# Performance work log

Measured on AMD Instinct MI355X. Metric: run time of the kernel, lower is better.

## Reference

```python
import jax, jax.numpy as jnp
import numpy as np

EPS = 1e-6
NEG = 0.2  # leaky-relu negative slope
OBJ_C = 6

def _knn(x, k):
    # x: [B,3,N] -> [B,N,k] indices of k nearest neighbors (incl. self)
    xx = jnp.sum(x * x, axis=1)
    inner = jnp.einsum('bdn,bdm->bnm', x, x)
    pd = 2.0 * inner - xx[:, :, None] - xx[:, None, :]  # negative sq dist
    return jax.lax.top_k(pd, k)[1]

def _gather_pts(xt, idx):
    # xt [B,N,D], idx [B,N,k] -> [B,N,k,D]
    return xt[jnp.arange(xt.shape[0])[:, None, None], idx]

def _vn_lin(W, x):
    # channel-mixing linear over VN channel dim: x [B,Cin,3,...]
    return jnp.einsum('oc,bc...->bo...', W, x)

def _vn_bn(x, g, b, eps=1e-5):
    # VNBatchNorm with batch statistics on vector norms
    n = jnp.linalg.norm(x, axis=2) + EPS          # [B,C,*spatial]
    axes = (0,) + tuple(range(2, n.ndim))
    m = jnp.mean(n, axes, keepdims=True)
    v = jnp.var(n, axes, keepdims=True)
    shp = (1, -1) + (1,) * (n.ndim - 2)
    nb = g.reshape(shp) * (n - m) / jnp.sqrt(v + eps) + b.reshape(shp)
    return x / n[:, :, None] * nb[:, :, None]

def _vn_leaky(p, d):
    dot = jnp.sum(p * d, axis=2, keepdims=True)
    dsq = jnp.sum(d * d, axis=2, keepdims=True)
    return NEG * p + (1.0 - NEG) * jnp.where(dot >= 0, p, p - (dot / (dsq + EPS)) * d)

def _vn_block(x, wf, wd, g=None, b=None):
    # VNLinearLeakyReLU
    p = _vn_lin(wf, x)
    if g is not None:
        p = _vn_bn(p, g, b)
    return _vn_leaky(p, _vn_lin(wd, x))

def _surface_feature(coord, k):
    # coord [B,3,N] -> [B,3(chan),3(vec),N,k]: (nb-ctr, ctr, nb x ctr)
    idx = _knn(coord, k)
    xt = coord.transpose(0, 2, 1)                                  # [B,N,3]
    nb = _gather_pts(xt, idx)[:, :, :, None, :]                    # [B,N,k,1,3]
    ctr = jnp.broadcast_to(xt[:, :, None, None, :], nb.shape)
    f = jnp.concatenate([nb - ctr, ctr, jnp.cross(nb, ctr, axis=-1)], axis=3)
    return f.transpose(0, 3, 4, 1, 2)

def _neighbor_feature(x, coord, k):
    # x [B,C,3,N], knn over coord -> [B,C,3,N,k]
    B, C, _, N = x.shape
    idx = _knn(coord, k)
    xt = x.reshape(B, C * 3, N).transpose(0, 2, 1)                 # [B,N,C*3]
    f = _gather_pts(xt, idx).reshape(B, N, k, C, 3)
    return f.transpose(0, 3, 4, 1, 2)

def _vn_maxpool_down(x, coord, wd, rate):
    # x [B,C,3,N,k]: stride-subsample points, VN-max over k neighbors
    x = x[:, :, :, ::rate, :]
    coord_d = coord[:, :, ::rate]
    dot = jnp.sum(x * _vn_lin(wd, x), axis=2)                      # [B,C,Nd,k]
    idx = jnp.argmax(dot, axis=-1)
    xm = jnp.take_along_axis(x, idx[:, :, None, :, None], axis=-1)[..., 0]
    return xm, coord_d

def _nearest_index(t, s):
    # t [B,N,3], s [B,M,3] -> argmin sq-dist index [B,N]
    d = jnp.sum(t * t, -1)[:, :, None] - 2.0 * jnp.einsum('bnd,bmd->bnm', t, s) + jnp.sum(s * s, -1)[:, None, :]
    return jnp.argmin(d, axis=-1)

def _index_points(x, idx):
    # x [B,C,3,M], idx [B,N] -> [B,C,3,N]
    xt = x.transpose(0, 3, 1, 2)
    return xt[jnp.arange(x.shape[0])[:, None], idx].transpose(0, 2, 3, 1)

def _conv_bn_relu(x, w, b, g, be, eps=1e-5):
    # 1x1 Conv1d + BatchNorm1d (batch stats) + ReLU
    y = jnp.einsum('oc,bcn->bon', w, x) + b[None, :, None]
    m = jnp.mean(y, (0, 2), keepdims=True)
    v = jnp.var(y, (0, 2), keepdims=True)
    return jax.nn.relu(g[None, :, None] * (y - m) / jnp.sqrt(v + eps) + be[None, :, None])

def _forward(x, norm, cat_id, wf0, wd0, g0, b0, wf1, wd1, g1, b1, wp1, wf2, wd2, g2, b2, wf3, wd3, g3, b3, wp2, wf4, wd4, g4, b4, wv1f, wv1d, wv2f, wv2d, w3, ws1, cb1, sg1, sb1, ws2, cb2, sg2, sb2, ws3, cb3, sg3, sb3):
    B, _, _, N = x.shape
    coord = x.reshape(B, 3, N)
    one_hot = jax.nn.one_hot(cat_id, OBJ_C, dtype=x.dtype)
    x0 = _vn_block(_surface_feature(coord, 20), wf0, wd0, g0, b0).mean(-1)   # [B,42,3,N]
    x1 = _vn_block(x0, wf1, wd1, g1, b1)
    x2, coord2 = _vn_maxpool_down(_neighbor_feature(x1, coord, 4), coord, wp1, 4)
    x2 = _vn_block(x2, wf2, wd2, g2, b2)                                     # [B,84,3,N/4]
    x3 = _vn_block(x2, wf3, wd3, g3, b3)
    x4, coord4 = _vn_maxpool_down(_neighbor_feature(x3, coord2, 4), coord2, wp2, 4)
    x4 = _vn_block(x4, wf4, wd4, g4, b4)                                     # [B,168,3,N/16]
    ct = coord.transpose(0, 2, 1)
    i1 = _nearest_index(ct, coord2.transpose(0, 2, 1))
    i2 = _nearest_index(ct, coord4.transpose(0, 2, 1))
    eqv = jnp.concatenate([x0, x1, _index_points(x2, i1), _index_points(x3, i1), _index_points(x4, i2)], axis=1)  # [B,420,3,N]
    mean_feat = eqv.mean(-1, keepdims=True)                                  # [B,420,3,1]
    z = _vn_block(mean_feat, wv1f, wv1d)
    z = _vn_block(z, wv2f, wv2d)
    z = jnp.einsum('bcvm,kc->bvkm', z, w3)                                   # [B,3,2,1]
    inv_gl = jnp.einsum('bijm,bjkm->bikm', mean_feat, z).reshape(B, -1, 1)   # [B,840,1]
    inv_0 = jnp.broadcast_to(inv_gl, (B, inv_gl.shape[1], N))
    inv_1 = jnp.sum(mean_feat * coord[:, None], axis=2)                      # [B,420,N]
    oh = jnp.broadcast_to(one_hot[:, :, None], (B, OBJ_C, N))
    inv = jnp.concatenate([norm, inv_0, inv_1, oh], axis=1)                  # [B,1267,N]
    inv = _conv_bn_relu(inv, ws1, cb1, sg1, sb1)
    inv = _conv_bn_relu(inv, ws2, cb2, sg2, sb2)
    inv = _conv_bn_relu(inv, ws3, cb3, sg3, sb3)                             # [B,420,N]
    return eqv, mean_feat, inv, inv_gl

def setup_inputs():
    key = jax.random.key(0)
    ki = iter(jax.random.split(key, 40))
    B, N, D = 4, 2048, 42
    def lin(o, c):
        return jax.random.normal(next(ki), (o, c), jnp.float32) / float(np.sqrt(c))
    inp = dict(
        x=jax.random.normal(next(ki), (B, 1, 3, N), jnp.float32),
        norm=jax.random.normal(next(ki), (B, 1, N), jnp.float32),
        cat_id=jax.random.randint(next(ki), (B,), 0, OBJ_C),
        wf0=lin(D, 3), wd0=lin(D, 3), g0=jnp.ones(D), b0=jnp.zeros(D),
        wf1=lin(D, D), wd1=lin(D, D), g1=jnp.ones(D), b1=jnp.zeros(D),
        wp1=lin(D, D),
        wf2=lin(2 * D, D), wd2=lin(2 * D, D), g2=jnp.ones(2 * D), b2=jnp.zeros(2 * D),
        wf3=lin(2 * D, 2 * D), wd3=lin(2 * D, 2 * D), g3=jnp.ones(2 * D), b3=jnp.zeros(2 * D),
        wp2=lin(2 * D, 2 * D),
        wf4=lin(4 * D, 2 * D), wd4=lin(4 * D, 2 * D), g4=jnp.ones(4 * D), b4=jnp.zeros(4 * D),
        wv1f=lin(5 * D, 10 * D), wv1d=lin(5 * D, 10 * D),
        wv2f=lin(2 * D, 5 * D), wv2d=lin(2 * D, 5 * D),
        w3=lin(2, 2 * D),
        ws1=lin(1024, 1267), cb1=jnp.zeros(1024), sg1=jnp.ones(1024), sb1=jnp.zeros(1024),
        ws2=lin(512, 1024), cb2=jnp.zeros(512), sg2=jnp.ones(512), sb2=jnp.zeros(512),
        ws3=lin(420, 512), cb3=jnp.zeros(420), sg3=jnp.ones(420), sb3=jnp.zeros(420),
    )
    return inp

def reference(x, norm, cat_id, wf0, wd0, g0, b0, wf1, wd1, g1, b1, wp1, wf2, wd2, g2, b2, wf3, wd3, g3, b3, wp2, wf4, wd4, g4, b4, wv1f, wv1d, wv2f, wv2d, w3, ws1, cb1, sg1, sb1, ws2, cb2, sg2, sb2, ws3, cb3, sg3, sb3):
    return _forward(x, norm, cat_id, wf0, wd0, g0, b0, wf1, wd1, g1, b1, wp1, wf2, wd2, g2, b2, wf3, wd3, g3, b3, wp2, wf4, wd4, g4, b4, wv1f, wv1d, wv2f, wv2d, w3, ws1, cb1, sg1, sb1, ws2, cb2, sg2, sb2, ws3, cb3, sg3, sb3)
```

## Files before the change

kernel.cpp:

```cpp
#include <hip/hip_runtime.h>
#include <hip/hip_bf16.h>
#include <cstdint>
#include <cstddef>

#define NTOT 2048
#define BTOT 4

typedef short bf16x8 __attribute__((ext_vector_type(8)));
typedef float f32x4 __attribute__((ext_vector_type(4)));

__device__ inline unsigned short f2b(float v) {
    __hip_bfloat16 h = __float2bfloat16(v);
    return *reinterpret_cast<unsigned short*>(&h);
}

static const size_t WS_IDX20 = 0;
static const size_t WS_X0    = 1638400;
static const size_t WS_X1    = 3702784;
static const size_t WS_XM2   = 5767168;
static const size_t WS_X2    = 6025216;
static const size_t WS_X3    = 6541312;
static const size_t WS_IDX42 = 7057408;
static const size_t WS_XM4   = 7059456;
static const size_t WS_X4    = 7188480;
static const size_t WS_I1    = 7446528;
static const size_t WS_I2    = 7454720;
static const size_t WS_MF    = 7462912;
static const size_t WS_INVGL = 7467952;
static const size_t WS_STATS = 7471312;
static const size_t WS_CST   = 7472992;
static const size_t WS_CB    = 7480320;
static const size_t WS_AB    = 7484416;
static const size_t WS_W0    = 7496704;
static const size_t WS_Z1    = 7497728;
static const size_t WS_Z2    = 7500288;
static const size_t WS_W2B   = 13378560;
static const size_t WS_W3B   = 13640704;
static const size_t WS_Y1B   = 0;
static const size_t WS_Y2T   = 7480320;
static const size_t WS_Y2B   = 4194304;
static const size_t WS_Y3T   = 13771776;

#define ZERO_SPAN_BYTES ((7476904 - 7462912) * 4)

#define ST0_OFF 0
#define ST1_OFF 84
#define ST2_OFF 168
#define ST3_OFF 336
#define ST4_OFF 504
#define CST1_OFF 0
#define CST2_OFF 2048
#define CST3_OFF 3072

#define OUT_EQV   0
#define OUT_MF    10321920
#define OUT_INV   10326960
#define OUT_INVGL 13767600

template <int SLOTS, int K, int NQ>
__global__ __launch_bounds__(256)
void knn_reg_kernel(const float* __restrict__ coord, int cand_stride, int q_stride,
                    int* __restrict__ out_idx, int q_cnt)
{
#pragma clang fp contract(off)
    constexpr int Q = SLOTS / 8;
    int b = blockIdx.y;
    int wave = threadIdx.x >> 6, lane = threadIdx.x & 63;
    int qbase = (blockIdx.x * 4 + wave) * NQ;
    if (qbase >= q_cnt) return;
    float qx[NQ], qy[NQ], qz[NQ], xxq[NQ];
#pragma unroll
    for (int u = 0; u < NQ; ++u) {
        int nq = (qbase + u) * q_stride;
        qx[u] = coord[(b * 3 + 0) * NTOT + nq];
        qy[u] = coord[(b * 3 + 1) * NTOT + nq];
        qz[u] = coord[(b * 3 + 2) * NTOT + nq];
        xxq[u] = qx[u] * qx[u] + qy[u] * qy[u] + qz[u] * qz[u];
    }
    float v[NQ][SLOTS];
#pragma unroll
    for (int j = 0; j < SLOTS; ++j) {
        int mo = (lane + 64 * j) * cand_stride;
        float cx = coord[(b * 3 + 0) * NTOT + mo];
        float cy = coord[(b * 3 + 1) * NTOT + mo];
        float cz = coord[(b * 3 + 2) * NTOT + mo];
        float xxc = cx * cx + cy * cy + cz * cz;
#pragma unroll
        for (int u = 0; u < NQ; ++u) {
            float inner = qx[u] * cx + qy[u] * cy + qz[u] * cz;
            v[u][j] = (2.0f * inner - xxq[u]) - xxc;
        }
    }
    float qv[NQ][Q]; int qj[NQ][Q];
#pragma unroll
    for (int u = 0; u < NQ; ++u)
#pragma unroll
        for (int qq = 0; qq < Q; ++qq) {
            float nv = v[u][qq * 8]; int nj = qq * 8;
#pragma unroll
            for (int j = 1; j < 8; ++j)
                if (v[u][qq * 8 + j] > nv) { nv = v[u][qq * 8 + j]; nj = qq * 8 + j; }
            qv[u][qq] = nv; qj[u][qq] = nj;
        }
#pragma clang loop unroll(disable)
    for (int kk = 0; kk < K; ++kk) {
        float bv[NQ]; int bm[NQ];
#pragma unroll
        for (int u = 0; u < NQ; ++u) {
            float tv = qv[u][0]; int tj = qj[u][0];
#pragma unroll
            for (int qq = 1; qq < Q; ++qq)
                if (qv[u][qq] > tv) { tv = qv[u][qq]; tj = qj[u][qq]; }
            bv[u] = tv; bm[u] = lane + 64 * tj;
        }
        for (int off = 32; off; off >>= 1) {
            float ov[NQ]; int om[NQ];
#pragma unroll
            for (int u = 0; u < NQ; ++u) {
                ov[u] = __shfl_down(bv[u], off);
                om[u] = __shfl_down(bm[u], off);
            }
#pragma unroll
            for (int u = 0; u < NQ; ++u)
                if (ov[u] > bv[u] || (ov[u] == bv[u] && om[u] < bm[u])) {
                    bv[u] = ov[u]; bm[u] = om[u];
                }
        }
#pragma unroll
        for (int u = 0; u < NQ; ++u) {
            int m_win = __builtin_amdgcn_readfirstlane(bm[u]);
            if (lane == 0)
                out_idx[((size_t)(b * q_cnt) + qbase + u) * K + kk] = m_win;
            int w_slot = m_win >> 6;
            bool isw = (lane == (m_win & 63));
#pragma unroll
            for (int qq = 0; qq < Q; ++qq) {
                if (qq == (w_slot >> 3)) {
#pragma unroll
                    for (int j = 0; j < 8; ++j)
                        if (qq * 8 + j == w_slot)
                            v[u][qq * 8 + j] = isw ? -3.4e38f : v[u][qq * 8 + j];
                    float nv = v[u][qq * 8]; int nj = qq * 8;
#pragma unroll
                    for (int j = 1; j < 8; ++j)
                        if (v[u][qq * 8 + j] > nv) { nv = v[u][qq * 8 + j]; nj = qq * 8 + j; }
                    qv[u][qq] = nv; qj[u][qq] = nj;
                }
            }
        }
    }
}

template <int SLOTS>
__global__ __launch_bounds__(256)
void nearest_reg_kernel(const float* __restrict__ coord, int cand_stride,
                        int* __restrict__ out)
{
#pragma clang fp contract(off)
    int b = blockIdx.y;
    int wave = threadIdx.x >> 6, lane = threadIdx.x & 63;
    int n = blockIdx.x * 4 + wave;
    float qx = coord[(b * 3 + 0) * NTOT + n];
    float qy = coord[(b * 3 + 1) * NTOT + n];
    float qz = coord[(b * 3 + 2) * NTOT + n];
    float tt = qx * qx + qy * qy + qz * qz;
    float v[SLOTS];
#pragma unroll
    for (int j = 0; j < SLOTS; ++j) {
        int mo = (lane + 64 * j) * cand_stride;
        float cx = coord[(b * 3 + 0) * NTOT + mo];
        float cy = coord[(b * 3 + 1) * NTOT + mo];
        float cz = coord[(b * 3 + 2) * NTOT + mo];
        float inner = qx * cx + qy * cy + qz * cz;
        float ss = cx * cx + cy * cy + cz * cz;
        v[j] = (tt - 2.0f * inner) + ss;
    }
    float bv = v[0];
    int bj = 0;
#pragma unroll
    for (int j = 1; j < SLOTS; ++j)
        if (v[j] < bv) { bv = v[j]; bj = j; }
    int bm = lane + 64 * bj;
    for (int off = 32; off; off >>= 1) {
        float ov = __shfl_down(bv, off);
        int   om = __shfl_down(bm, off);
        if (ov < bv || (ov == bv && om < bm)) { bv = ov; bm = om; }
    }
    if (lane == 0) out[b * NTOT + n] = bm;
}

__global__ __launch_bounds__(256)
void stats0_kernel(const float* __restrict__ coord, const int* __restrict__ idx20,
                   const float* __restrict__ wf0, double* __restrict__ stats)
{
    __shared__ float nbc[360];
    __shared__ float ctr[18];
    __shared__ double red[2][6][42];
    int t = threadIdx.x, b = blockIdx.y;
    int ps = t / 42, o = t - ps * 42;
    bool active = ps < 6;
    float w0 = 0.f, w1 = 0.f, w2 = 0.f;
    if (active) { w0 = wf0[o * 3]; w1 = wf0[o * 3 + 1]; w2 = wf0[o * 3 + 2]; }
    double s = 0.0, s2 = 0.0;
    int base = blockIdx.x * 48;
    for (int it = 0; it < 8; ++it) {
        int n0 = base + it * 6;
        __syncthreads();
        if (t < 120) {
            int pl = t / 20, k = t - pl * 20;
            int n = n0 + pl; if (n > NTOT - 1) n = NTOT - 1;
            int m = idx20[((size_t)(b * NTOT + n)) * 20 + k];
            nbc[t * 3 + 0] = coord[(b * 3 + 0) * NTOT + m];
            nbc[t * 3 + 1] = coord[(b * 3 + 1) * NTOT + m];
            nbc[t * 3 + 2] = coord[(b * 3 + 2) * NTOT + m];
        }
        if (t >= 128 && t < 146) {
            int i = t - 128; int pl = i / 3, vd = i - pl * 3;
            int n = n0 + pl; if (n > NTOT - 1) n = NTOT - 1;
            ctr[i] = coord[(b * 3 + vd) * NTOT + n];
        }
        __syncthreads();
        if (active && n0 + ps < NTOT) {
            float cx = ctr[ps * 3], cy = ctr[ps * 3 + 1], cz = ctr[ps * 3 + 2];
            const float* nb = &nbc[ps * 60];
            for (int k = 0; k < 20; ++k) {
                float nx = nb[k * 3], ny = nb[k * 3 + 1], nz = nb[k * 3 + 2];
                float dx = nx - cx, dy = ny - cy, dz = nz - cz;
                float crx = ny * cz - nz * cy;
                float cry = nz * cx - nx * cz;
                float crz = nx * cy - ny * cx;
                float p0 = w0 * dx + w1 * cx + w2 * crx;
                float p1 = w0 * dy + w1 * cy + w2 * cry;
                float p2 = w0 * dz + w1 * cz + w2 * crz;
                float nrm = sqrtf(p0 * p0 + p1 * p1 + p2 * p2) + 1e-6f;
                s += (double)nrm; s2 += (double)nrm * (double)nrm;
            }
        }
    }
    if (active) { red[0][ps][o] = s; red[1][ps][o] = s2; }
    __syncthreads();
    if (t < 42) {
        double a = 0.0, a2 = 0.0;
#pragma unroll
        for (int p = 0; p < 6; ++p) { a += red[0][p][t]; a2 += red[1][p][t]; }
        atomicAdd(&stats[t], a);
        atomicAdd(&stats[42 + t], a2);
    }
}

__global__ __launch_bounds__(256)
void apply0_kernel(const float* __restrict__ coord, const int* __restrict__ idx20,
                   const float* __restrict__ wf0, const float* __restrict__ wd0,
                   const float* __restrict__ g0, const float* __restrict__ b0,
                   const double* __restrict__ stats, float* __restrict__ x0)
{
    __shared__ float nbc[360];
    __shared__ float ctr[18];
    int t = threadIdx.x;
    int b = blockIdx.y;
    int ps = t / 42, o = t - ps * 42;
    int n0 = blockIdx.x * 6;
    if (t < 120) {
        int pl = t / 20, k = t - pl * 20;
        int n = n0 + pl; if (n > NTOT - 1) n = NTOT - 1;
        int m = idx20[((size_t)(b * NTOT + n)) * 20 + k];
        nbc[t * 3 + 0] = coord[(b * 3 + 0) * NTOT + m];
        nbc[t * 3 + 1] = coord[(b * 3 + 1) * NTOT + m];
        nbc[t * 3 + 2] = coord[(b * 3 + 2) * NTOT + m];
    }
    if (t >= 128 && t < 146) {
        int i = t - 128; int pl = i / 3, vd = i - pl * 3;
        int n = n0 + pl; if (n > NTOT - 1) n = NTOT - 1;
        ctr[i] = coord[(b * 3 + vd) * NTOT + n];
    }
    __syncthreads();
    int n = n0 + ps;
    if (ps >= 6 || n >= NTOT) return;
    double S1 = stats[o], S2 = stats[42 + o];
    double md = S1 / 163840.0;
    float m = (float)md;
    float var = (float)(S2 / 163840.0 - md * md);
    float gs = g0[o] / sqrtf(var + 1e-5f);
    float bb = b0[o];
    float wa0 = wf0[o * 3], wa1 = wf0[o * 3 + 1], wa2 = wf0[o * 3 + 2];
    float wb0 = wd0[o * 3], wb1 = wd0[o * 3 + 1], wb2 = wd0[o * 3 + 2];
    float cx = ctr[ps * 3], cy = ctr[ps * 3 + 1], cz = ctr[ps * 3 + 2];
    const float* nb = &nbc[ps * 60];
    float a0 = 0.f, a1 = 0.f, a2 = 0.f;
    for (int k = 0; k < 20; ++k) {
        float nx = nb[k * 3], ny = nb[k * 3 + 1], nz = nb[k * 3 + 2];
        float dx = nx - cx, dy = ny - cy, dz = nz - cz;
        float crx = ny * cz - nz * cy;
        float cry = nz * cx - nx * cz;
        float crz = nx * cy - ny * cx;
        float p0 = wa0 * dx + wa1 * cx + wa2 * crx;
        float p1 = wa0 * dy + wa1 * cy + wa2 * cry;
        float p2 = wa0 * dz + wa1 * cz + wa2 * crz;
        float d0 = wb0 * dx + wb1 * cx + wb2 * crx;
        float d1 = wb0 * dy + wb1 * cy + wb2 * cry;
        float d2 = wb0 * dz + wb1 * cz + wb2 * crz;
        float nrm = sqrtf(p0 * p0 + p1 * p1 + p2 * p2) + 1e-6f;
        float nbv = gs * (nrm - m) + bb;
        float sc = nbv / nrm;
        p0 *= sc; p1 *= sc; p2 *= sc;
        float dot = p0 * d0 + p1 * d1 + p2 * d2;
        float dsq = d0 * d0 + d1 * d1 + d2 * d2 + 1e-6f;
        float tq = fminf(dot, 0.f) / dsq;
        a0 += 0.2f * p0 + 0.8f * (p0 - tq * d0);
        a1 += 0.2f * p1 + 0.8f * (p1 - tq * d1);
        a2 += 0.2f * p2 + 0.8f * (p2 - tq * d2);
    }
    x0[((size_t)(b * 42 + o) * 3 + 0) * NTOT + n] = a0 / 20.0f;
    x0[((size_t)(b * 42 + o) * 3 + 1) * NTOT + n] = a1 / 20.0f;
    x0[((size_t)(b * 42 + o) * 3 + 2) * NTOT + n] = a2 / 20.0f;
}

template <int Ci, int Co, int PTS, int NT, int NIT>
__global__ __launch_bounds__(NT)
void vn_stats_kernel(const float* __restrict__ xin,
                     const float* __restrict__ wf,
                     double* __restrict__ stats, int Npts)
{
    constexpr int Ci3 = Ci * 3;
    constexpr int STRIDE = Ci3 + 1;
    __shared__ float col[PTS * STRIDE];
    __shared__ double red[2][PTS][Co];
    int t = threadIdx.x;
    int b = blockIdx.y;
    int ps = t / Co;
    int o = t - ps * Co;
    bool active = ps < PTS;
    double s = 0.0, s2 = 0.0;
    int base = blockIdx.x * (PTS * NIT);
    for (int it = 0; it < NIT; ++it) {
        int pt0 = base + it * PTS;
        __syncthreads();
        for (int i = t; i < PTS * Ci3; i += NT) {
            int pl = i / Ci3, off = i - pl * Ci3;
            int pt = pt0 + pl; if (pt >= Npts) pt = Npts - 1;
            col[pl * STRIDE + off] = xin[(size_t)(b * 3 * Ci + off) * Npts + pt];
        }
        __syncthreads();
        if (active && pt0 + ps < Npts) {
            const float* cl = &col[ps * STRIDE];
            const float* wr = wf + o * Ci;
            float p0 = 0.f, p1 = 0.f, p2 = 0.f;
#pragma unroll
            for (int c = 0; c < Ci; ++c) {
                float w = wr[c];
                p0 += w * cl[3 * c]; p1 += w * cl[3 * c + 1]; p2 += w * cl[3 * c + 2];
            }
            float nrm = sqrtf(p0 * p0 + p1 * p1 + p2 * p2) + 1e-6f;
            s += (double)nrm; s2 += (double)nrm * (double)nrm;
        }
    }
    if (active) { red[0][ps][o] = s; red[1][ps][o] = s2; }
    __syncthreads();
    if (t < Co) {
        double a = 0.0, a2 = 0.0;
#pragma unroll
        for (int p = 0; p < PTS; ++p) { a += red[0][p][t]; a2 += red[1][p][t]; }
        atomicAdd(&stats[t], a);
        atomicAdd(&stats[Co + t], a2);
    }
}

template <int Ci, int Co, int PTS, int NT>
__global__ __launch_bounds__(NT)
void vn_apply_kernel(const float* __restrict__ xin,
                     const float* __restrict__ wf,
                     const float* __restrict__ wd,
                     const float* __restrict__ g,
                     const float* __restrict__ bbp,
                     const double* __restrict__ stats,
                     double count, int Npts,
                     float* __restrict__ xout)
{
    constexpr int Ci3 = Ci * 3;
    constexpr int STRIDE = Ci3 + 1;
    __shared__ float col[PTS * STRIDE];
    int t = threadIdx.x;
    int b = blockIdx.y;
    int ps = t / Co;
    int o = t - ps * Co;
    bool active = ps < PTS;
    float m = 0.f, gs = 0.f, bb = 0.f;
    if (active) {
        double S1 = stats[o], S2 = stats[Co + o];
        double md = S1 / count;
        m = (float)md;
        float var = (float)(S2 / count - md * md);
        gs = g[o] / sqrtf(var + 1e-5f);
        bb = bbp[o];
    }
    int pt0 = blockIdx.x * PTS;
    for (int i = t; i < PTS * Ci3; i += NT) {
        int pl = i / Ci3, off = i - pl * Ci3;
        int pt = pt0 + pl; if (pt >= Npts) pt = Npts - 1;
        col[pl * STRIDE + off] = xin[(size_t)(b * 3 * Ci + off) * Npts + pt];
    }
    __syncthreads();
    int pt = pt0 + ps;
    if (!active || pt >= Npts) return;
    const float* cl = &col[ps * STRIDE];
    const float* wr = wf + o * Ci;
    const float* wdr = wd + o * Ci;
    float p0 = 0.f, p1 = 0.f, p2 = 0.f, d0 = 0.f, d1 = 0.f, d2 = 0.f;
#pragma unroll
    for (int c = 0; c < Ci; ++c) {
        float c0 = cl[3 * c], c1 = cl[3 * c + 1], c2 = cl[3 * c + 2];
        float w = wr[c];
        p0 += w * c0; p1 += w * c1; p2 += w * c2;
        float w2 = wdr[c];
        d0 += w2 * c0; d1 += w2 * c1; d2 += w2 * c2;
    }
    float nrm = sqrtf(p0 * p0 + p1 * p1 + p2 * p2) + 1e-6f;
    float nb = gs * (nrm - m) + bb;
    float sc = nb / nrm;
    p0 *= sc; p1 *= sc; p2 *= sc;
    float dot = p0 * d0 + p1 * d1 + p2 * d2;
    float dsq = d0 * d0 + d1 * d1 + d2 * d2 + 1e-6f;
    float tq = fminf(dot, 0.f) / dsq;
    float r0 = p0 - tq * d0, r1 = p1 - tq * d1, r2 = p2 - tq * d2;
    xout[((size_t)(b * Co + o) * 3 + 0) * Npts + pt] = 0.2f * p0 + 0.8f * r0;
    xout[((size_t)(b * Co + o) * 3 + 1) * Npts + pt] = 0.2f * p1 + 0.8f * r1;
    xout[((size_t)(b * Co + o) * 3 + 2) * Npts + pt] = 0.2f * p2 + 0.8f * r2;
}

__global__ void vn_pool_kernel(const float* __restrict__ xin,
                               const int* __restrict__ idx, long long sb, int sq,
                               const float* __restrict__ wp,
                               float* __restrict__ xout,
                               int C, int Np, int Nq)
{
#pragma clang fp contract(off)
    __shared__ float nb[4 * 84 * 3];
    int b = blockIdx.y;
    int q = blockIdx.x;
    const int* ir = idx + b * sb + (long long)q * sq;
    for (int kk = 0; kk < 4; ++kk) {
        int mm = ir[kk];
        for (int t = threadIdx.x; t < C * 3; t += blockDim.x)
            nb[kk * C * 3 + t] = xin[(size_t)(b * 3 * C + t) * Np + mm];
    }
    __syncthreads();
    int o = threadIdx.x;
    if (o >= C) return;
    const float* wr = wp + o * C;
    float best = -3.4e38f;
    int bk = 0;
    for (int kk = 0; kk < 4; ++kk) {
        const float* cl = &nb[kk * C * 3];
        float d0 = 0.f, d1 = 0.f, d2 = 0.f;
        for (int c = 0; c < C; ++c) {
            float w = wr[c];
            d0 += w * cl[3 * c]; d1 += w * cl[3 * c + 1]; d2 += w * cl[3 * c + 2];
        }
        float dot = cl[o * 3] * d0 + cl[o * 3 + 1] * d1 + cl[o * 3 + 2] * d2;
        if (dot > best) { best = dot; bk = kk; }
    }
    const float* cb = &nb[bk * C * 3];
    xout[((size_t)(b * C + o) * 3 + 0) * Nq + q] = cb[o * 3];
    xout[((size_t)(b * C + o) * 3 + 1) * Nq + q] = cb[o * 3 + 1];
    xout[((size_t)(b * C + o) * 3 + 2) * Nq + q] = cb[o * 3 + 2];
}

__global__ void eqv_kernel(const float* __restrict__ x0, const float* __restrict__ x1,
                           const float* __restrict__ x2, const float* __restrict__ x3,
                           const float* __restrict__ x4,
                           const int* __restrict__ i1, const int* __restrict__ i2,
                           float* __restrict__ out_eqv, float* __restrict__ mfw)
{
    __shared__ float wsum[4];
    int n = blockIdx.x * 256 + threadIdx.x;
    int cv = blockIdx.y;
    int b = blockIdx.z;
    int cc = cv / 3, v = cv % 3;
    float val;
    if (cc < 42)
        val = x0[((size_t)(b * 42 + cc) * 3 + v) * NTOT + n];
    else if (cc < 84)
        val = x1[((size_t)(b * 42 + (cc - 42)) * 3 + v) * NTOT + n];
    else if (cc < 168) {
        int m = i1[b * NTOT + n];
        val = x2[((size_t)(b * 84 + (cc - 84)) * 3 + v) * 512 + m];
    } else if (cc < 252) {
        int m = i1[b * NTOT + n];
        val = x3[((size_t)(b * 84 + (cc - 168)) * 3 + v) * 512 + m];
    } else {
        int m = i2[b * NTOT + n];
        val = x4[((size_t)(b * 168 + (cc - 252)) * 3 + v) * 128 + m];
    }
    out_eqv[((size_t)(b * 1260 + cv)) * NTOT + n] = val;
    float s = val;
    for (int off = 32; off; off >>= 1) s += __shfl_down(s, off);
    if ((threadIdx.x & 63) == 0) wsum[threadIdx.x >> 6] = s;
    __syncthreads();
    if (threadIdx.x == 0)
        atomicAdd(&mfw[b * 1260 + cv], (wsum[0] + wsum[1]) + (wsum[2] + wsum[3]));
}

__global__ void mf_finalize_kernel(float* __restrict__ mfw, float* __restrict__ out_mf)
{
    int i = blockIdx.x * 256 + threadIdx.x;
    if (i < 5040) {
        float m = mfw[i] / 2048.0f;
        mfw[i] = m;
        out_mf[i] = m;
    }
}

__global__ __launch_bounds__(256)
void z1_kernel(const float* __restrict__ mfw,
               const float* __restrict__ wv1f, const float* __restrict__ wv1d,
               float* __restrict__ z1ws)
{
    __shared__ float mf[1260];
    int b = blockIdx.y;
    int wave = threadIdx.x >> 6, lane = threadIdx.x & 63;
    for (int i = threadIdx.x; i < 1260; i += 256) mf[i] = mfw[b * 1260 + i];
    __syncthreads();
    int o = blockIdx.x * 4 + wave;
    if (o >= 210) return;
    const float* wr  = wv1f + (size_t)o * 420;
    const float* wdr = wv1d + (size_t)o * 420;
    float p0 = 0.f, p1 = 0.f, p2 = 0.f, d0 = 0.f, d1 = 0.f, d2 = 0.f;
    for (int c = lane; c < 420; c += 64) {
        float m0 = mf[3 * c], m1 = mf[3 * c + 1], m2 = mf[3 * c + 2];
        float w = wr[c];
        p0 += w * m0; p1 += w * m1; p2 += w * m2;
        float w2 = wdr[c];
        d0 += w2 * m0; d1 += w2 * m1; d2 += w2 * m2;
    }
    for (int off = 32; off; off >>= 1) {
        p0 += __shfl_down(p0, off); p1 += __shfl_down(p1, off);
        p2 += __shfl_down(p2, off); d0 += __shfl_down(d0, off);
        d1 += __shfl_down(d1, off); d2 += __shfl_down(d2, off);
    }
    if (lane == 0) {
        float dot = p0 * d0 + p1 * d1 + p2 * d2;
        float r0, r1, r2;
        if (dot >= 0.f) { r0 = p0; r1 = p1; r2 = p2; }
        else {
            float tq = dot / (d0 * d0 + d1 * d1 + d2 * d2 + 1e-6f);
            r0 = p0 - tq * d0; r1 = p1 - tq * d1; r2 = p2 - tq * d2;
        }
        z1ws[b * 630 + o * 3]     = 0.2f * p0 + 0.8f * r0;
        z1ws[b * 630 + o * 3 + 1] = 0.2f * p1 + 0.8f * r1;
        z1ws[b * 630 + o * 3 + 2] = 0.2f * p2 + 0.8f * r2;
    }
}

__global__ __launch_bounds__(256)
void z2_kernel(const float* __restrict__ z1ws,
               const float* __restrict__ wv2f, const float* __restrict__ wv2d,
               float* __restrict__ z2ws)
{
    __shared__ float zl[630];
    int b = blockIdx.y;
    int wave = threadIdx.x >> 6, lane = threadIdx.x & 63;
    for (int i = threadIdx.x; i < 630; i += 256) zl[i] = z1ws[b * 630 + i];
    __syncthreads();
    int o = blockIdx.x * 4 + wave;
    if (o >= 84) return;
    const float* wr  = wv2f + (size_t)o * 210;
    const float* wdr = wv2d + (size_t)o * 210;
    float p0 = 0.f, p1 = 0.f, p2 = 0.f, d0 = 0.f, d1 = 0.f, d2 = 0.f;
    for (int c = lane; c < 210; c += 64) {
        float m0 = zl[3 * c], m1 = zl[3 * c + 1], m2 = zl[3 * c + 2];
        float w = wr[c];
        p0 += w * m0; p1 += w * m1; p2 += w * m2;
        float w2 = wdr[c];
        d0 += w2 * m0; d1 += w2 * m1; d2 += w2 * m2;
    }
    for (int off = 32; off; off >>= 1) {
        p0 += __shfl_down(p0, off); p1 += __shfl_down(p1, off);
        p2 += __shfl_down(p2, off); d0 += __shfl_down(d0, off);
        d1 += __shfl_down(d1, off); d2 += __shfl_down(d2, off);
    }
    if (lane == 0) {
        float dot = p0 * d0 + p1 * d1 + p2 * d2;
        float r0, r1, r2;
        if (dot >= 0.f) { r0 = p0; r1 = p1; r2 = p2; }
        else {
            float tq = dot / (d0 * d0 + d1 * d1 + d2 * d2 + 1e-6f);
            r0 = p0 - tq * d0; r1 = p1 - tq * d1; r2 = p2 - tq * d2;
        }
        z2ws[b * 252 + o * 3]     = 0.2f * p0 + 0.8f * r0;
        z2ws[b * 252 + o * 3 + 1] = 0.2f * p1 + 0.8f * r1;
        z2ws[b * 252 + o * 3 + 2] = 0.2f * p2 + 0.8f * r2;
    }
}

__global__ void z3invgl_kernel(const float* __restrict__ mfw,
                               const float* __restrict__ z2ws,
                               const float* __restrict__ w3,
                               float* __restrict__ invgl_ws,
                               float* __restrict__ out_invgl)
{
    __shared__ float z2[252];
    __shared__ float z3[6];
    __shared__ float mf[1260];
    int b = blockIdx.x;
    int t = threadIdx.x;
    for (int i = t; i < 252; i += 256) z2[i] = z2ws[b * 252 + i];
    for (int i = t; i < 1260; i += 256) mf[i] = mfw[b * 1260 + i];
    __syncthreads();
    if (t < 6) {
        int v = t / 2, kt = t % 2;
        float s = 0.f;
        for (int c = 0; c < 84; ++c) s += z2[c * 3 + v] * w3[kt * 84 + c];
        z3[v * 2 + kt] = s;
    }
    __syncthreads();
    for (int i = t; i < 840; i += 256) {
        int ii = i / 2, kt = i % 2;
        float s = mf[ii * 3] * z3[0 + kt] + mf[ii * 3 + 1] * z3[2 + kt] +
                  mf[ii * 3 + 2] * z3[4 + kt];
        invgl_ws[b * 840 + i] = s;
        out_invgl[b * 840 + i] = s;
    }
}

__global__ __launch_bounds__(256)
void conv1_coef_kernel(const float* __restrict__ ws1,
                       const float* __restrict__ invgl,
                       const float* __restrict__ mfw,
                       const int* __restrict__ cat,
                       float* __restrict__ cb, float* __restrict__ ab,
                       float* __restrict__ w0)
{
    int wave = threadIdx.x >> 6, lane = threadIdx.x & 63;
    int o = blockIdx.x * 4 + wave;
    int b = blockIdx.y;
    const float* wr = ws1 + (size_t)o * 1267;
    float s = 0.f;
    for (int j = lane; j < 840; j += 64)
        s += wr[1 + j] * invgl[b * 840 + j];
    float a0 = 0.f, a1 = 0.f, a2 = 0.f;
    for (int i = lane; i < 420; i += 64) {
        float w = wr[841 + i];
        a0 += w * mfw[b * 1260 + i * 3];
        a1 += w * mfw[b * 1260 + i * 3 + 1];
        a2 += w * mfw[b * 1260 + i * 3 + 2];
    }
    for (int off = 32; off; off >>= 1) {
        s  += __shfl_down(s, off);
        a0 += __shfl_down(a0, off);
        a1 += __shfl_down(a1, off);
        a2 += __shfl_down(a2, off);
    }
    if (lane == 0) {
        cb[b * 1024 + o] = s + wr[1261 + cat[b]];
        ab[((size_t)(b * 1024 + o)) * 3 + 0] = a0;
        ab[((size_t)(b * 1024 + o)) * 3 + 1] = a1;
        ab[((size_t)(b * 1024 + o)) * 3 + 2] = a2;
        if (b == 0) w0[o] = wr[0];
    }
}

__global__ __launch_bounds__(256)
void y1_stats_kernel(const float* __restrict__ cb, const float* __restrict__ ab,
                     const float* __restrict__ w0, const float* __restrict__ coord,
                     const float* __restrict__ normv, float* __restrict__ cst)
{
    __shared__ float px[256], py[256], pz[256], pn[256];
    int t = threadIdx.x;
    int o = blockIdx.x * 256 + t;
    int b = blockIdx.y >> 3;
    int n0 = (blockIdx.y & 7) * 256;
    px[t] = coord[(b * 3 + 0) * NTOT + n0 + t];
    py[t] = coord[(b * 3 + 1) * NTOT + n0 + t];
    pz[t] = coord[(b * 3 + 2) * NTOT + n0 + t];
    pn[t] = normv[b * NTOT + n0 + t];
    __syncthreads();
    size_t bo = (size_t)(b * 1024 + o);
    float c0 = cb[bo];
    float a0 = ab[bo * 3], a1 = ab[bo * 3 + 1], a2 = ab[bo * 3 + 2];
    float wn = w0[o];
    float s = 0.f, s2 = 0.f;
    for (int k = 0; k < 256; ++k) {
        float v = c0 + a0 * px[k] + a1 * py[k] + a2 * pz[k] + wn * pn[k];
        s += v; s2 += v * v;
    }
    atomicAdd(&cst[o], s);
    atomicAdd(&cst[1024 + o], s2);
}

__global__ __launch_bounds__(256)
void y1_bnrelu_kernel(const float* __restrict__ cb, const float* __restrict__ ab,
                      const float* __restrict__ w0, const float* __restrict__ coord,
                      const float* __restrict__ normv, const float* __restrict__ cst,
                      const float* __restrict__ sg, const float* __restrict__ sb,
                      unsigned short* __restrict__ y1b)
{
    __shared__ float px[256], py[256], pz[256], pn[256];
    int t = threadIdx.x;
    int o = blockIdx.x * 256 + t;
    int b = blockIdx.y >> 3;
    int n0 = (blockIdx.y & 7) * 256;
    px[t] = coord[(b * 3 + 0) * NTOT + n0 + t];
    py[t] = coord[(b * 3 + 1) * NTOT + n0 + t];
    pz[t] = coord[(b * 3 + 2) * NTOT + n0 + t];
    pn[t] = normv[b * NTOT + n0 + t];
    __syncthreads();
    size_t bo = (size_t)(b * 1024 + o);
    float c0 = cb[bo];
    float a0 = ab[bo * 3], a1 = ab[bo * 3 + 1], a2 = ab[bo * 3 + 2];
    float wn = w0[o];
    float mm = cst[o] * (1.f / 8192.f);
    float var = cst[1024 + o] * (1.f / 8192.f) - mm * mm;
    float sc = sg[o] / sqrtf(var + 1e-5f);
    float bs = sb[o] - mm * sc;
    size_t rowbase = (size_t)(b * NTOT + n0) * 1024 + o;
    for (int k = 0; k < 256; ++k) {
        float v = c0 + a0 * px[k] + a1 * py[k] + a2 * pz[k] + wn * pn[k];
        float r = sc * v + bs;
        y1b[rowbase + (size_t)k * 1024] = f2b(r > 0.f ? r : 0.f);
    }
}

__global__ void wconv_kernel(const float* __restrict__ src, unsigned short* __restrict__ dst,
                             int Msrc, int Ksrc, int Kpad)
{
    int k = blockIdx.x * 256 + threadIdx.x;
    int o = blockIdx.y;
    float v = (o < Msrc && k < Ksrc) ? src[(size_t)o * Ksrc + k] : 0.f;
    dst[(size_t)o * Kpad + k] = f2b(v);
}

__global__ __launch_bounds__(256)
void gemm_mfma_kernel(const unsigned short* __restrict__ A,
                      const unsigned short* __restrict__ Bw,
                      float* __restrict__ C, float* __restrict__ st,
                      int K, int Mreal)
{
    __shared__ __align__(16) unsigned short Al[64 * 72];
    __shared__ __align__(16) unsigned short Bl[64 * 72];
    __shared__ float sst[64], sst2[64];
    int t = threadIdx.x;
    if (t < 64) { sst[t] = 0.f; sst2[t] = 0.f; }
    int r0 = blockIdx.x * 64;
    int c0 = blockIdx.y * 64;
    int w = t >> 6, l = t & 63;
    int wm = w & 1, wn = w >> 1;
    int lm = l & 15, lq = l >> 4;
    f32x4 acc[2][2] = {};
    for (int k0 = 0; k0 < K; k0 += 64) {
#pragma unroll
        for (int half = 0; half < 2; ++half) {
            int ch = t + half * 256;
            int row = ch >> 3, kc = ch & 7;
            *(uint4*)&Al[row * 72 + kc * 8] =
                *(const uint4*)&A[(size_t)(r0 + row) * K + k0 + kc * 8];
            *(uint4*)&Bl[row * 72 + kc * 8] =
                *(const uint4*)&Bw[(size_t)(c0 + row) * K + k0 + kc * 8];
        }
        __syncthreads();
        bf16x8 af[2][2], bfr[2][2];
#pragma unroll
        for (int kk = 0; kk < 2; ++kk) {
#pragma unroll
            for (int i = 0; i < 2; ++i)
                af[kk][i] = *(const bf16x8*)&Al[(wm * 32 + i * 16 + lm) * 72 + kk * 32 + lq * 8];
#pragma unroll
            for (int j = 0; j < 2; ++j)
                bfr[kk][j] = *(const bf16x8*)&Bl[(wn * 32 + j * 16 + lm) * 72 + kk * 32 + lq * 8];
        }
#pragma unroll
        for (int kk = 0; kk < 2; ++kk)
#pragma unroll
            for (int i = 0; i < 2; ++i)
#pragma unroll
                for (int j = 0; j < 2; ++j)
                    acc[i][j] = __builtin_amdgcn_mfma_f32_16x16x32_bf16(
                        af[kk][i], bfr[kk][j], acc[i][j], 0, 0, 0);
        __syncthreads();
    }
#pragma unroll
    for (int i = 0; i < 2; ++i) {
#pragma unroll
        for (int j = 0; j < 2; ++j) {
            int col = c0 + wn * 32 + j * 16 + lm;
            if (col < Mreal) {
                int rbase = r0 + wm * 32 + i * 16 + lq * 4;
#pragma unroll
                for (int r = 0; r < 4; ++r)
                    C[(size_t)(rbase + r) * Mreal + col] = acc[i][j][r];
            }
        }
    }
#pragma unroll
    for (int j = 0; j < 2; ++j) {
        float s = 0.f, s2 = 0.f;
#pragma unroll
        for (int i = 0; i < 2; ++i)
#pragma unroll
            for (int r = 0; r < 4; ++r) { float x = acc[i][j][r]; s += x; s2 += x * x; }
        s  += __shfl_down(s, 32);  s  += __shfl_down(s, 16);
        s2 += __shfl_down(s2, 32); s2 += __shfl_down(s2, 16);
        if (l < 16) {
            int cc = wn * 32 + j * 16 + lm;
            atomicAdd(&sst[cc], s);
            atomicAdd(&sst2[cc], s2);
        }
    }
    __syncthreads();
    if (t < 64) {
        int col = c0 + t;
        if (col < Mreal) {
            atomicAdd(&st[col], sst[t]);
            atomicAdd(&st[Mreal + col], sst2[t]);
        }
    }
}

__global__ void bnreluT_kernel(const float* __restrict__ Ct, const float* __restrict__ st,
                               const float* __restrict__ g, const float* __restrict__ be,
                               unsigned short* __restrict__ outb, int M, int maskM)
{
    size_t idx = (size_t)blockIdx.x * 256 + threadIdx.x;
    int o = (int)(idx & (size_t)maskM);
    float m = st[o] * (1.f / 8192.f);
    float var = st[M + o] * (1.f / 8192.f) - m * m;
    float sqv = sqrtf(var + 1e-5f);
    float v = g[o] * (Ct[idx] - m) / sqv + be[o];
    outb[idx] = f2b(v > 0.f ? v : 0.f);
}

__global__ void bnrelu_outT_kernel(const float* __restrict__ Ct, const float* __restrict__ st,
                                   const float* __restrict__ g, const float* __restrict__ be,
                                   float* __restrict__ outinv)
{
    __shared__ float tile[64][65];
    int t = threadIdx.x;
    int r0 = blockIdx.x * 64;
    int o0 = blockIdx.y * 64;
    int b = r0 >> 11, n0 = r0 & 2047;
    int oi = t & 63;
    int o = o0 + oi;
    float m = 0.f, sqv = 1.f, gg = 0.f, bb = 0.f;
    if (o < 420) {
        m = st[o] * (1.f / 8192.f);
        float var = st[420 + o] * (1.f / 8192.f) - m * m;
        sqv = sqrtf(var + 1e-5f);
        gg = g[o]; bb = be[o];
    }
    for (int it = 0; it < 16; ++it) {
        int rr = it * 4 + (t >> 6);
        float v = 0.f;
        if (o < 420) {
            v = gg * (Ct[(size_t)(r0 + rr) * 420 + o] - m) / sqv + bb;
            v = v > 0.f ? v : 0.f;
        }
        tile[rr][oi] = v;
    }
    __syncthreads();
    for (int it = 0; it < 16; ++it) {
        int oc = it * 4 + (t >> 6);
        int oo = o0 + oc;
        if (oo < 420)
            outinv[((size_t)(b * 420 + oo)) * 2048 + n0 + (t & 63)] = tile[t & 63][oc];
    }
}

extern "C" void kernel_launch(void* const* d_in, const int* in_sizes, int n_in,
                              void* d_out, int out_size, void* d_ws, size_t ws_size,
                              hipStream_t stream)
{
    (void)in_sizes; (void)n_in; (void)out_size; (void)ws_size;
    const float* xc   = (const float*)d_in[0];
    const float* normv= (const float*)d_in[1];
    const int*   cat  = (const int*)d_in[2];
    const float* wf0  = (const float*)d_in[3];
    const float* wd0  = (const float*)d_in[4];
    const float* g0   = (const float*)d_in[5];
    const float* b0   = (const float*)d_in[6];
    const float* wf1  = (const float*)d_in[7];
    const float* wd1  = (const float*)d_in[8];
    const float* g1   = (const float*)d_in[9];
    const float* b1   = (const float*)d_in[10];
    const float* wp1  = (const float*)d_in[11];
    const float* wf2  = (const float*)d_in[12];
    const float* wd2  = (const float*)d_in[13];
    const float* g2   = (const float*)d_in[14];
    const float* b2   = (const float*)d_in[15];
    const float* wf3  = (const float*)d_in[16];
    const float* wd3  = (const float*)d_in[17];
    const float* g3   = (const float*)d_in[18];
    const float* b3   = (const float*)d_in[19];
    const float* wp2  = (const float*)d_in[20];
    const float* wf4  = (const float*)d_in[21];
    const float* wd4  = (const float*)d_in[22];
    const float* g4   = (const float*)d_in[23];
    const float* b4   = (const float*)d_in[24];
    const float* wv1f = (const float*)d_in[25];
    const float* wv1d = (const float*)d_in[26];
    const float* wv2f = (const float*)d_in[27];
    const float* wv2d = (const float*)d_in[28];
    const float* w3   = (const float*)d_in[29];
    const float* ws1  = (const float*)d_in[30];
    const float* sg1  = (const float*)d_in[32];
    const float* sb1  = (const float*)d_in[33];
    const float* ws2  = (const float*)d_in[34];
    const float* sg2  = (const float*)d_in[36];
    const float* sb2  = (const float*)d_in[37];
    const float* ws3  = (const float*)d_in[38];
    const float* sg3  = (const float*)d_in[40];
    const float* sb3  = (const float*)d_in[41];

    float* ws = (float*)d_ws;
    float* out = (float*)d_out;

    int*    idx20 = (int*)(ws + WS_IDX20);
    float*  x0    = ws + WS_X0;
    float*  x1    = ws + WS_X1;
    float*  xm2   = ws + WS_XM2;
    float*  x2    = ws + WS_X2;
    float*  x3    = ws + WS_X3;
    int*    idx42 = (int*)(ws + WS_IDX42);
    float*  xm4   = ws + WS_XM4;
    float*  x4    = ws + WS_X4;
    int*    i1p   = (int*)(ws + WS_I1);
    int*    i2p   = (int*)(ws + WS_I2);
    float*  mfw   = ws + WS_MF;
    float*  invgl = ws + WS_INVGL;
    double* st    = (double*)(ws + WS_STATS);
    float*  cst   = ws + WS_CST;
    float*  cb    = ws + WS_CB;
    float*  ab    = ws + WS_AB;
    float*  w0    = ws + WS_W0;
    float*  z1ws  = ws + WS_Z1;
    float*  z2ws  = ws + WS_Z2;
    unsigned short* w2b  = (unsigned short*)(ws + WS_W2B);
    unsigned short* w3b  = (unsigned short*)(ws + WS_W3B);
    unsigned short* y1b  = (unsigned short*)(ws + WS_Y1B);
    float*  y2t   = ws + WS_Y2T;
    unsigned short* y2b  = (unsigned short*)(ws + WS_Y2B);
    float*  y3t   = ws + WS_Y3T;

    hipMemsetAsync((void*)mfw, 0, ZERO_SPAN_BYTES, stream);

    wconv_kernel<<<dim3(4, 512), 256, 0, stream>>>(ws2, w2b, 512, 1024, 1024);
    wconv_kernel<<<dim3(2, 512), 256, 0, stream>>>(ws3, w3b, 420, 512, 512);

    knn_reg_kernel<32, 20, 2><<<dim3(256, 4), 256, 0, stream>>>(xc, 1, 1, idx20, 2048);

    stats0_kernel<<<dim3(43, 4), 256, 0, stream>>>(xc, idx20, wf0, st + ST0_OFF);
    apply0_kernel<<<dim3(342, 4), 256, 0, stream>>>(xc, idx20, wf0, wd0, g0, b0,
                                                    st + ST0_OFF, x0);

    vn_stats_kernel<42, 42, 6, 256, 8><<<dim3(43, 4), 256, 0, stream>>>(
        x0, wf1, st + ST1_OFF, 2048);
    vn_apply_kernel<42, 42, 6, 256><<<dim3(342, 4), 256, 0, stream>>>(
        x0, wf1, wd1, g1, b1, st + ST1_OFF, 8192.0, 2048, x1);

    vn_pool_kernel<<<dim3(512, 4), 256, 0, stream>>>(x1, idx20, 40960LL, 80, wp1, xm2,
                                                     42, 2048, 512);
    vn_stats_kernel<42, 84, 3, 256, 8><<<dim3(22, 4), 256, 0, stream>>>(
        xm2, wf2, st + ST2_OFF, 512);
    vn_apply_kernel<42, 84, 3, 256><<<dim3(171, 4), 256, 0, stream>>>(
        xm2, wf2, wd2, g2, b2, st + ST2_OFF, 2048.0, 512, x2);
    vn_stats_kernel<84, 84, 3, 256, 8><<<dim3(22, 4), 256, 0, stream>>>(
        x2, wf3, st + ST3_OFF, 512);
    vn_apply_kernel<84, 84, 3, 256><<<dim3(171, 4), 256, 0, stream>>>(
        x2, wf3, wd3, g3, b3, st + ST3_OFF, 2048.0, 512, x3);

    knn_reg_kernel<8, 4, 1><<<dim3(32, 4), 256, 0, stream>>>(xc, 4, 16, idx42, 128);
    vn_pool_kernel<<<dim3(128, 4), 256, 0, stream>>>(x3, idx42, 512LL, 4, wp2, xm4,
                                                     84, 512, 128);
    vn_stats_kernel<84, 168, 3, 512, 4><<<dim3(11, 4), 512, 0, stream>>>(
        xm4, wf4, st + ST4_OFF, 128);
    vn_apply_kernel<84, 168, 3, 512><<<dim3(43, 4), 512, 0, stream>>>(
        xm4, wf4, wd4, g4, b4, st + ST4_OFF, 512.0, 128, x4);

    nearest_reg_kernel<8><<<dim3(512, 4), 256, 0, stream>>>(xc, 4, i1p);
    nearest_reg_kernel<2><<<dim3(512, 4), 256, 0, stream>>>(xc, 16, i2p);

    eqv_kernel<<<dim3(8, 1260, 4), 256, 0, stream>>>(x0, x1, x2, x3, x4, i1p, i2p,
                                                     out + OUT_EQV, mfw);
    mf_finalize_kernel<<<20, 256, 0, stream>>>(mfw, out + OUT_MF);

    z1_kernel<<<dim3(53, 4), 256, 0, stream>>>(mfw, wv1f, wv1d, z1ws);
    z2_kernel<<<dim3(21, 4), 256, 0, stream>>>(z1ws, wv2f, wv2d, z2ws);
    z3invgl_kernel<<<4, 256, 0, stream>>>(mfw, z2ws, w3, invgl, out + OUT_INVGL);

    conv1_coef_kernel<<<dim3(256, 4), 256, 0, stream>>>(ws1, invgl, mfw, cat, cb, ab, w0);
    y1_stats_kernel<<<dim3(4, 32), 256, 0, stream>>>(cb, ab, w0, xc, normv,
                                                     cst + CST1_OFF);
    y1_bnrelu_kernel<<<dim3(4, 32), 256, 0, stream>>>(cb, ab, w0, xc, normv,
                                                      cst + CST1_OFF, sg1, sb1, y1b);

    gemm_mfma_kernel<<<dim3(128, 8), 256, 0, stream>>>(y1b, w2b, y2t, cst + CST2_OFF,
                                                       1024, 512);
    bnreluT_kernel<<<16384, 256, 0, stream>>>(y2t, cst + CST2_OFF, sg2, sb2, y2b,
                                              512, 511);

    gemm_mfma_kernel<<<dim3(128, 7), 256, 0, stream>>>(y2b, w3b, y3t, cst + CST3_OFF,
                                                       512, 420);
    bnrelu_outT_kernel<<<dim3(128, 7), 256, 0, stream>>>(y3t, cst + CST3_OFF, sg3, sb3,
                                                         out + OUT_INV);
}
```

Before: 577.1 us.

## Add point-major copies for pooling gathers, fuse nearest kernels, use float inner sums

The VN apply kernels for layers 1 and 3 now also write a point-major transposed copy of their output, so vn_pool can gather each neighbour's channels contiguously instead of with strided reads. The two nearest-neighbour kernels are merged into one that derives the stride-16 argmin from the stride-4 candidates it already loaded. stats0 accumulates the per-point norm sums in float and converts to double once per point rather than per neighbour. The cost is extra global writes for the transposed buffers and slightly lower precision in the stats0 partial sums.

New measurement: 585.8 us, median of 2. No clear change (+1.5%).

```diff
diff --git a/kernel.cpp b/kernel.cpp
--- a/kernel.cpp
+++ b/kernel.cpp
@@ -15,6 +15,7 @@
 }
 
 static const size_t WS_IDX20 = 0;
+static const size_t WS_X1T   = 163840;
 static const size_t WS_X0    = 1638400;
 static const size_t WS_X1    = 3702784;
 static const size_t WS_XM2   = 5767168;
@@ -34,6 +35,7 @@
 static const size_t WS_W0    = 7496704;
 static const size_t WS_Z1    = 7497728;
 static const size_t WS_Z2    = 7500288;
+static const size_t WS_X3T   = 7501312;
 static const size_t WS_W2B   = 13378560;
 static const size_t WS_W3B   = 13640704;
 static const size_t WS_Y1B   = 0;
@@ -151,10 +153,9 @@
     }
 }
 
-template <int SLOTS>
 __global__ __launch_bounds__(256)
-void nearest_reg_kernel(const float* __restrict__ coord, int cand_stride,
-                        int* __restrict__ out)
+void nearest_dual_kernel(const float* __restrict__ coord,
+                         int* __restrict__ out1, int* __restrict__ out2)
 {
 #pragma clang fp contract(off)
     int b = blockIdx.y;
@@ -164,10 +165,10 @@
     float qy = coord[(b * 3 + 1) * NTOT + n];
     float qz = coord[(b * 3 + 2) * NTOT + n];
     float tt = qx * qx + qy * qy + qz * qz;
-    float v[SLOTS];
-#pragma unroll
-    for (int j = 0; j < SLOTS; ++j) {
-        int mo = (lane + 64 * j) * cand_stride;
+    float v[8];
+#pragma unroll
+    for (int j = 0; j < 8; ++j) {
+        int mo = (lane + 64 * j) * 4;
         float cx = coord[(b * 3 + 0) * NTOT + mo];
         float cy = coord[(b * 3 + 1) * NTOT + mo];
         float cz = coord[(b * 3 + 2) * NTOT + mo];
@@ -178,15 +179,31 @@
     float bv = v[0];
     int bj = 0;
 #pragma unroll
-    for (int j = 1; j < SLOTS; ++j)
+    for (int j = 1; j < 8; ++j)
         if (v[j] < bv) { bv = v[j]; bj = j; }
     int bm = lane + 64 * bj;
+    bool has2 = ((lane & 3) == 0);
+    float bv2 = 3.4e38f;
+    int bm2 = 0x7fffffff;
+    if (has2) {
+        bv2 = v[0]; bm2 = (lane >> 2);
+#pragma unroll
+        for (int j = 1; j < 8; ++j) {
+            if (v[j] < bv2) { bv2 = v[j]; bm2 = (lane >> 2) + 16 * j; }
+        }
+    }
     for (int off = 32; off; off >>= 1) {
         float ov = __shfl_down(bv, off);
         int   om = __shfl_down(bm, off);
         if (ov < bv || (ov == bv && om < bm)) { bv = ov; bm = om; }
-    }
-    if (lane == 0) out[b * NTOT + n] = bm;
+        float ov2 = __shfl_down(bv2, off);
+        int   om2 = __shfl_down(bm2, off);
+        if (ov2 < bv2 || (ov2 == bv2 && om2 < bm2)) { bv2 = ov2; bm2 = om2; }
+    }
+    if (lane == 0) {
+        out1[b * NTOT + n] = bm;
+        out2[b * NTOT + n] = bm2;
+    }
 }
 
 __global__ __launch_bounds__(256)
@@ -223,6 +240,7 @@
         if (active && n0 + ps < NTOT) {
             float cx = ctr[ps * 3], cy = ctr[ps * 3 + 1], cz = ctr[ps * 3 + 2];
             const float* nb = &nbc[ps * 60];
+            float sf = 0.f, sf2 = 0.f;
             for (int k = 0; k < 20; ++k) {
                 float nx = nb[k * 3], ny = nb[k * 3 + 1], nz = nb[k * 3 + 2];
                 float dx = nx - cx, dy = ny - cy, dz = nz - cz;
@@ -233,8 +251,9 @@
                 float p1 = w0 * dy + w1 * cy + w2 * cry;
                 float p2 = w0 * dz + w1 * cz + w2 * crz;
                 float nrm = sqrtf(p0 * p0 + p1 * p1 + p2 * p2) + 1e-6f;
-                s += (double)nrm; s2 += (double)nrm * (double)nrm;
+                sf += nrm; sf2 += nrm * nrm;
             }
+            s += (double)sf; s2 += (double)sf2;
         }
     }
     if (active) { red[0][ps][o] = s; red[1][ps][o] = s2; }
@@ -365,7 +384,7 @@
     }
 }
 
-template <int Ci, int Co, int PTS, int NT>
+template <int Ci, int Co, int PTS, int NT, bool WT>
 __global__ __launch_bounds__(NT)
 void vn_apply_kernel(const float* __restrict__ xin,
                      const float* __restrict__ wf,
@@ -374,10 +393,12 @@
                      const float* __restrict__ bbp,
                      const double* __restrict__ stats,
                      double count, int Npts,
-                     float* __restrict__ xout)
+                     float* __restrict__ xout,
+                     float* __restrict__ xt)
 {
     constexpr int Ci3 = Ci * 3;
     constexpr int STRIDE = Ci3 + 1;
+    constexpr int CH = Co * 3;
     __shared__ float col[PTS * STRIDE];
     int t = threadIdx.x;
     int b = blockIdx.y;
@@ -422,12 +443,19 @@
     float dsq = d0 * d0 + d1 * d1 + d2 * d2 + 1e-6f;
     float tq = fminf(dot, 0.f) / dsq;
     float r0 = p0 - tq * d0, r1 = p1 - tq * d1, r2 = p2 - tq * d2;
-    xout[((size_t)(b * Co + o) * 3 + 0) * Npts + pt] = 0.2f * p0 + 0.8f * r0;
-    xout[((size_t)(b * Co + o) * 3 + 1) * Npts + pt] = 0.2f * p1 + 0.8f * r1;
-    xout[((size_t)(b * Co + o) * 3 + 2) * Npts + pt] = 0.2f * p2 + 0.8f * r2;
-}
-
-__global__ void vn_pool_kernel(const float* __restrict__ xin,
+    float o0 = 0.2f * p0 + 0.8f * r0;
+    float o1 = 0.2f * p1 + 0.8f * r1;
+    float o2 = 0.2f * p2 + 0.8f * r2;
+    xout[((size_t)(b * Co + o) * 3 + 0) * Npts + pt] = o0;
+    xout[((size_t)(b * Co + o) * 3 + 1) * Npts + pt] = o1;
+    xout[((size_t)(b * Co + o) * 3 + 2) * Npts + pt] = o2;
+    if (WT) {
+        float* tp = xt + ((size_t)(b * Npts + pt)) * CH + o * 3;
+        tp[0] = o0; tp[1] = o1; tp[2] = o2;
+    }
+}
+
+__global__ void vn_pool_kernel(const float* __restrict__ xint,
                                const int* __restrict__ idx, long long sb, int sq,
                                const float* __restrict__ wp,
                                float* __restrict__ xout,
@@ -438,10 +466,12 @@
     int b = blockIdx.y;
     int q = blockIdx.x;
     const int* ir = idx + b * sb + (long long)q * sq;
+    int CH = C * 3;
     for (int kk = 0; kk < 4; ++kk) {
         int mm = ir[kk];
-        for (int t = threadIdx.x; t < C * 3; t += blockDim.x)
-            nb[kk * C * 3 + t] = xin[(size_t)(b * 3 * C + t) * Np + mm];
+        const float* src = xint + ((size_t)(b * Np + mm)) * CH;
+        for (int t = threadIdx.x; t < CH; t += blockDim.x)
+            nb[kk * CH + t] = src[t];
     }
     __syncthreads();
     int o = threadIdx.x;
@@ -450,7 +480,7 @@
     float best = -3.4e38f;
     int bk = 0;
     for (int kk = 0; kk < 4; ++kk) {
-        const float* cl = &nb[kk * C * 3];
+        const float* cl = &nb[kk * CH];
         float d0 = 0.f, d1 = 0.f, d2 = 0.f;
         for (int c = 0; c < C; ++c) {
             float w = wr[c];
@@ -459,7 +489,7 @@
         float dot = cl[o * 3] * d0 + cl[o * 3 + 1] * d1 + cl[o * 3 + 2] * d2;
         if (dot > best) { best = dot; bk = kk; }
     }
-    const float* cb = &nb[bk * C * 3];
+    const float* cb = &nb[bk * CH];
     xout[((size_t)(b * C + o) * 3 + 0) * Nq + q] = cb[o * 3];
     xout[((size_t)(b * C + o) * 3 + 1) * Nq + q] = cb[o * 3 + 1];
     xout[((size_t)(b * C + o) * 3 + 2) * Nq + q] = cb[o * 3 + 2];
@@ -913,6 +943,7 @@
     float* out = (float*)d_out;
 
     int*    idx20 = (int*)(ws + WS_IDX20);
+    float*  x1t   = ws + WS_X1T;
     float*  x0    = ws + WS_X0;
     float*  x1    = ws + WS_X1;
     float*  xm2   = ws + WS_XM2;
@@ -932,6 +963,7 @@
     float*  w0    = ws + WS_W0;
     float*  z1ws  = ws + WS_Z1;
     float*  z2ws  = ws + WS_Z2;
+    float*  x3t   = ws + WS_X3T;
     unsigned short* w2b  = (unsigned short*)(ws + WS_W2B);
     unsigned short* w3b  = (unsigned short*)(ws + WS_W3B);
     unsigned short* y1b  = (unsigned short*)(ws + WS_Y1B);
@@ -952,30 +984,29 @@
 
     vn_stats_kernel<42, 42, 6, 256, 8><<<dim3(43, 4), 256, 0, stream>>>(
         x0, wf1, st + ST1_OFF, 2048);
-    vn_apply_kernel<42, 42, 6, 256><<<dim3(342, 4), 256, 0, stream>>>(
-        x0, wf1, wd1, g1, b1, st + ST1_OFF, 8192.0, 2048, x1);
-
-    vn_pool_kernel<<<dim3(512, 4), 256, 0, stream>>>(x1, idx20, 40960LL, 80, wp1, xm2,
+    vn_apply_kernel<42, 42, 6, 256, true><<<dim3(342, 4), 256, 0, stream>>>(
+        x0, wf1, wd1, g1, b1, st + ST1_OFF, 8192.0, 2048, x1, x1t);
+
+    vn_pool_kernel<<<dim3(512, 4), 256, 0, stream>>>(x1t, idx20, 40960LL, 80, wp1, xm2,
                                                      42, 2048, 512);
     vn_stats_kernel<42, 84, 3, 256, 8><<<dim3(22, 4), 256, 0, stream>>>(
         xm2, wf2, st + ST2_OFF, 512);
-    vn_apply_kernel<42, 84, 3, 256><<<dim3(171, 4), 256, 0, stream>>>(
-        xm2, wf2, wd2, g2, b2, st + ST2_OFF, 2048.0, 512, x2);
+    vn_apply_kernel<42, 84, 3, 256, false><<<dim3(171, 4), 256, 0, stream>>>(
+        xm2, wf2, wd2, g2, b2, st + ST2_OFF, 2048.0, 512, x2, nullptr);
     vn_stats_kernel<84, 84, 3, 256, 8><<<dim3(22, 4), 256, 0, stream>>>(
         x2, wf3, st + ST3_OFF, 512);
-    vn_apply_kernel<84, 84, 3, 256><<<dim3(171, 4), 256, 0, stream>>>(
-        x2, wf3, wd3, g3, b3, st + ST3_OFF, 2048.0, 512, x3);
+    vn_apply_kernel<84, 84, 3, 256, true><<<dim3(171, 4), 256, 0, stream>>>(
+        x2, wf3, wd3, g3, b3, st + ST3_OFF, 2048.0, 512, x3, x3t);
 
     knn_reg_kernel<8, 4, 1><<<dim3(32, 4), 256, 0, stream>>>(xc, 4, 16, idx42, 128);
-    vn_pool_kernel<<<dim3(128, 4), 256, 0, stream>>>(x3, idx42, 512LL, 4, wp2, xm4,
+    vn_pool_kernel<<<dim3(128, 4), 256, 0, stream>>>(x3t, idx42, 512LL, 4, wp2, xm4,
                                                      84, 512, 128);
     vn_stats_kernel<84, 168, 3, 512, 4><<<dim3(11, 4), 512, 0, stream>>>(
         xm4, wf4, st + ST4_OFF, 128);
-    vn_apply_kernel<84, 168, 3, 512><<<dim3(43, 4), 512, 0, stream>>>(
-        xm4, wf4, wd4, g4, b4, st + ST4_OFF, 512.0, 128, x4);
-
-    nearest_reg_kernel<8><<<dim3(512, 4), 256, 0, stream>>>(xc, 4, i1p);
-    nearest_reg_kernel<2><<<dim3(512, 4), 256, 0, stream>>>(xc, 16, i2p);
+    vn_apply_kernel<84, 168, 3, 512, false><<<dim3(43, 4), 512, 0, stream>>>(
+        xm4, wf4, wd4, g4, b4, st + ST4_OFF, 512.0, 128, x4, nullptr);
+
+    nearest_dual_kernel<<<dim3(512, 4), 256, 0, stream>>>(xc, i1p, i2p);
 
     eqv_kernel<<<dim3(8, 1260, 4), 256, 0, stream>>>(x0, x1, x2, x3, x4, i1p, i2p,
                                                      out + OUT_EQV, mfw);
```
